# Kernel tuning notes

Hardware: AMD Instinct MI355X
Metric: run time of the kernel (lower is better)

The kernel has to match this reference:

```python
import jax, jax.numpy as jnp
import numpy as np

BATCH, N_FIELDS, EMBED, OUT = 32768, 64, 128, 10


def setup_inputs() -> dict:
    key = jax.random.key(0)
    kx, kw = jax.random.split(key)
    x = jax.random.normal(kx, (BATCH, N_FIELDS, EMBED), dtype=jnp.float32)
    # Xavier uniform for weights of shape (output_size, n_fields)
    limit = float(np.sqrt(6.0 / (OUT + N_FIELDS)))
    weights = jax.random.uniform(kw, (OUT, N_FIELDS), dtype=jnp.float32,
                                 minval=-limit, maxval=limit)
    return {"x": x, "weights": weights}


def reference(x, weights):
    # delta[r,p,f,e] = x[r,f,e] * w[p,f]; ip[r,p] = sum_{f,e} delta^2
    # Algebraically: ip[r,p] = sum_f w[p,f]^2 * sum_e x[r,f,e]^2
    x_sq = jnp.sum(x * x, axis=-1)            # [batch, n_fields]
    ip = jnp.einsum('rf,pf->rp', x_sq, weights * weights)  # [batch, output_size]
    return ip
```

## Files before the change

### kernel.cpp

```cpp
#include <hip/hip_runtime.h>


#define BATCH   32768
#define NF      64
#define EMBED   128
#define OUT_N   10
#define ROW_F   (NF * EMBED)
#define W2_PAD  12

__global__ __launch_bounds__(256) void ip_kernel(
    const float* __restrict__ x,
    const float* __restrict__ w,
    float* __restrict__ out)
{
    __shared__ float w2[NF * W2_PAD];
    for (int i = threadIdx.x; i < OUT_N * NF; i += 256) {
        int p = i >> 6;
        int f = i & 63;
        float v = w[i];
        w2[f * W2_PAD + p] = v * v;
    }
    __syncthreads();

    const int lane = threadIdx.x & 63;
    const int wid  = threadIdx.x >> 6;
    const int row  = blockIdx.x * 4 + wid;

    const float4* __restrict__ base =
        (const float4*)(x + (size_t)row * ROW_F);

    float acc[OUT_N];
    #pragma unroll
    for (int p = 0; p < OUT_N; ++p) acc[p] = 0.0f;

    const int half = lane >> 5;

    #pragma unroll 8
    for (int t = 0; t < 32; ++t) {
        float4 v = base[t * 64 + lane];
        float s = v.x * v.x + v.y * v.y + v.z * v.z + v.w * v.w;

        const float4* wr4 = (const float4*)&w2[(2 * t + half) * W2_PAD];
        float4 w0 = wr4[0];
        float4 w1 = wr4[1];
        float4 w2v = wr4[2];

        acc[0] += s * w0.x;  acc[1] += s * w0.y;
        acc[2] += s * w0.z;  acc[3] += s * w0.w;
        acc[4] += s * w1.x;  acc[5] += s * w1.y;
        acc[6] += s * w1.z;  acc[7] += s * w1.w;
        acc[8] += s * w2v.x; acc[9] += s * w2v.y;
    }

    #pragma unroll
    for (int off = 32; off >= 1; off >>= 1) {
        #pragma unroll
        for (int p = 0; p < OUT_N; ++p)
            acc[p] += __shfl_xor(acc[p], off, 64);
    }

    if (lane == 0) {
        float* o = out + (size_t)row * OUT_N;
        #pragma unroll
        for (int p = 0; p < OUT_N; ++p) o[p] = acc[p];
    }
}

extern "C" void kernel_launch(void* const* d_in, const int* in_sizes, int n_in,
                              void* d_out, int out_size, void* d_ws, size_t ws_size,
                              hipStream_t stream) {
    const float* x = (const float*)d_in[0];
    const float* w = (const float*)d_in[1];
    float* out = (float*)d_out;

    dim3 grid(BATCH / 4);
    dim3 block(256);
    ip_kernel<<<grid, block, 0, stream>>>(x, w, out);
}
```

Measured before the change: 1.308 ms.

## Process four rows per wavefront with nontemporal loads and shared weight reads

```diff
diff --git a/kernel.cpp b/kernel.cpp
--- a/kernel.cpp
+++ b/kernel.cpp
@@ -1,12 +1,18 @@
 #include <hip/hip_runtime.h>
 
+
+typedef float f4 __attribute__((ext_vector_type(4)));
+typedef float f2 __attribute__((ext_vector_type(2)));
 
 #define BATCH   32768
 #define NF      64
 #define EMBED   128
 #define OUT_N   10
 #define ROW_F   (NF * EMBED)
+#define ROW_F4  (ROW_F / 4)
 #define W2_PAD  12
+#define RPW     4
+#define RPB     16
 
 __global__ __launch_bounds__(256) void ip_kernel(
     const float* __restrict__ x,
@@ -24,45 +30,63 @@
 
     const int lane = threadIdx.x & 63;
     const int wid  = threadIdx.x >> 6;
-    const int row  = blockIdx.x * 4 + wid;
-
-    const float4* __restrict__ base =
-        (const float4*)(x + (size_t)row * ROW_F);
-
-    float acc[OUT_N];
-    #pragma unroll
-    for (int p = 0; p < OUT_N; ++p) acc[p] = 0.0f;
-
     const int half = lane >> 5;
 
-    #pragma unroll 8
+    const size_t row0 = (size_t)blockIdx.x * RPB + (size_t)wid * RPW;
+    const f4* __restrict__ base = (const f4*)(x + row0 * ROW_F);
+
+    float acc[RPW][OUT_N];
+    #pragma unroll
+    for (int r = 0; r < RPW; ++r)
+        #pragma unroll
+        for (int p = 0; p < OUT_N; ++p) acc[r][p] = 0.0f;
+
+    #pragma unroll 2
     for (int t = 0; t < 32; ++t) {
-        float4 v = base[t * 64 + lane];
-        float s = v.x * v.x + v.y * v.y + v.z * v.z + v.w * v.w;
+        f4 v0 = __builtin_nontemporal_load(&base[0 * ROW_F4 + t * 64 + lane]);
+        f4 v1 = __builtin_nontemporal_load(&base[1 * ROW_F4 + t * 64 + lane]);
+        f4 v2 = __builtin_nontemporal_load(&base[2 * ROW_F4 + t * 64 + lane]);
+        f4 v3 = __builtin_nontemporal_load(&base[3 * ROW_F4 + t * 64 + lane]);
 
-        const float4* wr4 = (const float4*)&w2[(2 * t + half) * W2_PAD];
-        float4 w0 = wr4[0];
-        float4 w1 = wr4[1];
-        float4 w2v = wr4[2];
+        const float* wrow = &w2[(2 * t + half) * W2_PAD];
+        f4 wa = *(const f4*)&wrow[0];
+        f4 wb = *(const f4*)&wrow[4];
+        f2 wc = *(const f2*)&wrow[8];
 
-        acc[0] += s * w0.x;  acc[1] += s * w0.y;
-        acc[2] += s * w0.z;  acc[3] += s * w0.w;
-        acc[4] += s * w1.x;  acc[5] += s * w1.y;
-        acc[6] += s * w1.z;  acc[7] += s * w1.w;
-        acc[8] += s * w2v.x; acc[9] += s * w2v.y;
+        float s0 = v0[0]*v0[0] + v0[1]*v0[1] + v0[2]*v0[2] + v0[3]*v0[3];
+        float s1 = v1[0]*v1[0] + v1[1]*v1[1] + v1[2]*v1[2] + v1[3]*v1[3];
+        float s2 = v2[0]*v2[0] + v2[1]*v2[1] + v2[2]*v2[2] + v2[3]*v2[3];
+        float s3 = v3[0]*v3[0] + v3[1]*v3[1] + v3[2]*v3[2] + v3[3]*v3[3];
+
+        #define APPLY(r, sv)                                    \
+            acc[r][0] += (sv) * wa[0]; acc[r][1] += (sv) * wa[1]; \
+            acc[r][2] += (sv) * wa[2]; acc[r][3] += (sv) * wa[3]; \
+            acc[r][4] += (sv) * wb[0]; acc[r][5] += (sv) * wb[1]; \
+            acc[r][6] += (sv) * wb[2]; acc[r][7] += (sv) * wb[3]; \
+            acc[r][8] += (sv) * wc[0]; acc[r][9] += (sv) * wc[1];
+        APPLY(0, s0)
+        APPLY(1, s1)
+        APPLY(2, s2)
+        APPLY(3, s3)
+        #undef APPLY
     }
 
     #pragma unroll
     for (int off = 32; off >= 1; off >>= 1) {
         #pragma unroll
-        for (int p = 0; p < OUT_N; ++p)
-            acc[p] += __shfl_xor(acc[p], off, 64);
+        for (int r = 0; r < RPW; ++r)
+            #pragma unroll
+            for (int p = 0; p < OUT_N; ++p)
+                acc[r][p] += __shfl_xor(acc[r][p], off, 64);
     }
 
     if (lane == 0) {
-        float* o = out + (size_t)row * OUT_N;
         #pragma unroll
-        for (int p = 0; p < OUT_N; ++p) o[p] = acc[p];
+        for (int r = 0; r < RPW; ++r) {
+            float* o = out + (row0 + r) * OUT_N;
+            #pragma unroll
+            for (int p = 0; p < OUT_N; ++p) o[p] = acc[r][p];
+        }
     }
 }
 
@@ -73,7 +97,7 @@
     const float* w = (const float*)d_in[1];
     float* out = (float*)d_out;
 
-    dim3 grid(BATCH / 4);
+    dim3 grid(BATCH / RPB);
     dim3 block(256);
     ip_kernel<<<grid, block, 0, stream>>>(x, w, out);
 }
```

Measured after the change: 1.303 ms. Within noise of the previous version (-0.4%).
